# Kernel optimization log

Measured on AMD Instinct MI355X. Metric: run time of the kernel, lower is better.

## Reference

```python
import jax, jax.numpy as jnp
import numpy as np

D = 128  # hard-coded hidden dim in MLP_T

def setup_inputs() -> dict:
    key = jax.random.key(0)
    ks = jax.random.split(key, 8)
    N, IN = 16384, 768
    return {
        "x": jax.random.normal(ks[0], (N, IN), dtype=jnp.float32),
        "decay_value": 1,
        "W_token": jax.random.normal(ks[1], (IN, D), dtype=jnp.float32) * (IN ** -0.5),
        "b_token": jax.random.normal(ks[2], (D,), dtype=jnp.float32) * 0.02,
        "W_qkv": jax.random.normal(ks[3], (D, 3 * D), dtype=jnp.float32) * (D ** -0.5),
        "b_qkv": jax.random.normal(ks[4], (3 * D,), dtype=jnp.float32) * 0.02,
        "W_fc": jax.random.normal(ks[5], (D, 1), dtype=jnp.float32) * (D ** -0.5),
        "b_fc": jax.random.normal(ks[6], (1,), dtype=jnp.float32) * 0.02,
    }

def reference(x, decay_value, W_token, b_token, W_qkv, b_qkv, W_fc, b_fc):
    # token projection: [N, in_chan] -> [N, 128]
    h = x @ W_token + b_token
    # qkv: [N, 384] split along feature dim into q, k, v of [N, 128]
    qkv = h @ W_qkv + b_qkv
    q, k, v = qkv[:, :D], qkv[:, D:2 * D], qkv[:, 2 * D:]
    # sigmoid attention (no row normalization); dropout is identity in eval mode
    att_scores = jax.nn.sigmoid(q @ k.T)            # [N, N]
    att = att_scores @ v                            # [N, 128]
    out = att @ W_fc + b_fc                         # [N, 1]
    # GradientReversal is identity in the forward pass
    return out
```

## Files before the change

### kernel.cpp

```cpp
#include <hip/hip_runtime.h>
#include <hip/hip_bf16.h>
#include <stdint.h>

#define N_ROWS 16384

typedef __bf16 bf16x8 __attribute__((ext_vector_type(8)));
typedef float f32x4 __attribute__((ext_vector_type(4)));

#define AS1 __attribute__((address_space(1)))
#define AS3 __attribute__((address_space(3)))

#define OFF_WCP  0u
#define OFF_BC   589824u
#define OFF_QB   591360u
#define OFF_KB   4785664u
#define OFF_WV   8979968u
#define OFF_PART 9045504u

__global__ void prep(const float* __restrict__ Wt, const float* __restrict__ Wq,
                     const float* __restrict__ bt, const float* __restrict__ bq,
                     __bf16* __restrict__ WcP, float* __restrict__ bc) {
    int u = blockIdx.x * 256 + threadIdx.x;
    if (u < 768 * 96) {
        int k = u / 96, n4 = u % 96;
        float s[4] = {0, 0, 0, 0};
        const float* wtp = Wt + k * 128;
        const float* wqp = Wq + n4 * 4;
#pragma unroll 8
        for (int d = 0; d < 128; d++) {
            float a = wtp[d];
            float4 b = *(const float4*)(wqp + d * 384);
            s[0] += a * b.x; s[1] += a * b.y; s[2] += a * b.z; s[3] += a * b.w;
        }
        int kbi = k >> 6, j = (k >> 3) & 7, k7 = k & 7;
#pragma unroll
        for (int jj = 0; jj < 4; jj++) {
            int n = n4 * 4 + jj;
            int sr = n >> 1, b = n & 1;
            WcP[kbi * 24576 + sr * 128 + (b * 8 + (j ^ (sr & 7))) * 8 + k7] = (__bf16)s[jj];
        }
    }
    if (u < 384) {
        float s = bq[u];
        for (int d = 0; d < 128; d++) s += bt[d] * Wq[d * 384 + u];
        bc[u] = s;
    }
}

__launch_bounds__(128)
__global__ void gemm_qkv(const float* __restrict__ x, const __bf16* __restrict__ WcP,
                         const float* __restrict__ bc, const float* __restrict__ W_fc,
                         __bf16* __restrict__ qb, __bf16* __restrict__ kb,
                         float* __restrict__ wv) {
    __shared__ float  Asm_[32 * 64];
    __shared__ __bf16 Bsm[384 * 64];
    const int tid = threadIdx.x, wave = tid >> 6, lane = tid & 63;
    const int n16 = lane & 15, q = lane >> 4;
    const int row0 = blockIdx.x * 32;

    const char* asrc[4];
#pragma unroll
    for (int ii = 0; ii < 4; ii++) {
        int r = wave * 16 + ii * 4 + (lane >> 4);
        int cp = lane & 15;
        int c = 2 * ((cp >> 1) ^ (r & 7)) + ((cp & 1) ^ ((r >> 3) & 1));
        asrc[ii] = (const char*)(x + (size_t)(row0 + r) * 768 + c * 4);
    }
    const char* bsrc = (const char*)WcP + (size_t)wave * 24576 + lane * 16;

    f32x4 acc[24];
#pragma unroll
    for (int t = 0; t < 24; t++) acc[t] = (f32x4){0, 0, 0, 0};

    const int rA = wave * 16 + n16;
    const int sa = rA & 7, hb = (rA >> 3) & 1;
    const int bbase = (n16 >> 1) * 256 + (n16 & 1) * 128;
    const int sb = (n16 >> 1) & 7;

    for (int kbi = 0; kbi < 12; kbi++) {
#pragma unroll
        for (int ii = 0; ii < 4; ii++)
            __builtin_amdgcn_global_load_lds((const AS1 void*)(asrc[ii] + kbi * 256),
                (AS3 void*)((char*)Asm_ + (wave * 4 + ii) * 1024 + lane * 16), 16, 0, 0);
#pragma unroll
        for (int ii = 0; ii < 24; ii++)
            __builtin_amdgcn_global_load_lds((const AS1 void*)(bsrc + (size_t)kbi * 49152 + ii * 1024),
                (AS3 void*)((char*)Bsm + (wave * 24 + ii) * 1024 + lane * 16), 16, 0, 0);
        __syncthreads();
#pragma unroll
        for (int ksub = 0; ksub < 2; ksub++) {
            const int P = ksub * 4 + q;
            const float* ap = Asm_ + rA * 64;
            f32x4 f0 = *(const f32x4*)(ap + (2 * (P ^ sa) + hb) * 4);
            f32x4 f1 = *(const f32x4*)(ap + (2 * (P ^ sa) + (1 ^ hb)) * 4);
            bf16x8 af;
            af[0] = (__bf16)f0[0]; af[1] = (__bf16)f0[1]; af[2] = (__bf16)f0[2]; af[3] = (__bf16)f0[3];
            af[4] = (__bf16)f1[0]; af[5] = (__bf16)f1[1]; af[6] = (__bf16)f1[2]; af[7] = (__bf16)f1[3];
            const char* bp = (const char*)Bsm + bbase + (P ^ sb) * 16 - (n16 & 1) * 128
                             + (n16 & 1) * 128;
            (void)bp;
#pragma unroll
            for (int t = 0; t < 24; t++) {
                const char* bpt = (const char*)Bsm + (n16 >> 1) * 256
                                  + ((n16 & 1) * 8 + (P ^ sb)) * 16 + t * 2048;
                bf16x8 bf = *(const bf16x8*)bpt;
                acc[t] = __builtin_amdgcn_mfma_f32_16x16x32_bf16(af, bf, acc[t], 0, 0, 0);
            }
        }
        __syncthreads();
    }

    float wacc[4] = {0, 0, 0, 0};
#pragma unroll
    for (int t = 0; t < 24; t++) {
        int col = t * 16 + n16;
        float bcv = bc[col];
        float wf = (t >= 16) ? W_fc[col - 256] : 0.0f;
#pragma unroll
        for (int r = 0; r < 4; r++) {
            int row = row0 + wave * 16 + q * 4 + r;
            float val = acc[t][r] + bcv;
            if (t < 8) {
                qb[row * 128 + col] = (__bf16)(val * -1.44269504088896f);
            } else if (t < 16) {
                int d = col - 128;
                kb[row * 128 + (((d >> 3) ^ (row & 15)) << 3) + (d & 7)] = (__bf16)val;
            } else {
                wacc[r] += val * wf;
            }
        }
    }
#pragma unroll
    for (int r = 0; r < 4; r++) {
        float v = wacc[r];
        v += __shfl_xor(v, 1, 64);
        v += __shfl_xor(v, 2, 64);
        v += __shfl_xor(v, 4, 64);
        v += __shfl_xor(v, 8, 64);
        if (n16 == 0) wv[row0 + wave * 16 + q * 4 + r] = v;
    }
}

__launch_bounds__(128)
__global__ void attn(const __bf16* __restrict__ qb, const __bf16* __restrict__ kb,
                     const float* __restrict__ wv, float* __restrict__ partial) {
    __shared__ __bf16 kbuf[64 * 128];
    __shared__ float wbuf[64];
    const int tid = threadIdx.x;
    const int wave = tid >> 6, lane = tid & 63;
    const int n16 = lane & 15, q = lane >> 4;
    const int row0 = blockIdx.x * 128 + wave * 64;
    const int sp = blockIdx.y;
    bf16x8 qf[4][4];
#pragma unroll
    for (int mt = 0; mt < 4; mt++)
#pragma unroll
        for (int ks = 0; ks < 4; ks++)
            qf[mt][ks] = *(const bf16x8*)(qb + (row0 + mt * 16 + n16) * 128 + ks * 32 + q * 8);
    float acc[4][4] = {{0}, {0}, {0}, {0}};
    for (int jc = 0; jc < 16; jc++) {
        const int jbase = sp * 1024 + jc * 64;
        const char* gsrc = (const char*)kb + (size_t)jbase * 256;
#pragma unroll
        for (int i = 0; i < 8; i++) {
            const int off = wave * 8192 + i * 1024;
            __builtin_amdgcn_global_load_lds(
                (const AS1 void*)(gsrc + off + lane * 16),
                (AS3 void*)((char*)kbuf + off), 16, 0, 0);
        }
        if (tid < 64) wbuf[tid] = wv[jbase + tid];
        __syncthreads();
#pragma unroll
        for (int t = 0; t < 4; t++) {
            f32x4 s[4];
#pragma unroll
            for (int mt = 0; mt < 4; mt++) s[mt] = (f32x4){0, 0, 0, 0};
#pragma unroll
            for (int ks = 0; ks < 4; ks++) {
                const int chunk = (ks * 4 + q) ^ n16;
                bf16x8 bf = *(const bf16x8*)(kbuf + (t * 16 + n16) * 128 + chunk * 8);
#pragma unroll
                for (int mt = 0; mt < 4; mt++)
                    s[mt] = __builtin_amdgcn_mfma_f32_16x16x32_bf16(qf[mt][ks], bf, s[mt], 0, 0, 0);
            }
            const float wval = wbuf[t * 16 + n16];
#pragma unroll
            for (int mt = 0; mt < 4; mt++)
#pragma unroll
                for (int r = 0; r < 4; r++)
                    acc[mt][r] += __builtin_amdgcn_rcpf(1.0f + __builtin_amdgcn_exp2f(s[mt][r])) * wval;
        }
        __syncthreads();
    }
#pragma unroll
    for (int mt = 0; mt < 4; mt++)
#pragma unroll
        for (int r = 0; r < 4; r++) {
            float v = acc[mt][r];
            v += __shfl_xor(v, 1, 64);
            v += __shfl_xor(v, 2, 64);
            v += __shfl_xor(v, 4, 64);
            v += __shfl_xor(v, 8, 64);
            if (n16 == 0) partial[sp * N_ROWS + row0 + mt * 16 + q * 4 + r] = v;
        }
}

__global__ void reduce_out(const float* __restrict__ partial, const float* __restrict__ b_fc,
                           float* __restrict__ out) {
    int i = blockIdx.x * 256 + threadIdx.x;
    float v = b_fc[0];
#pragma unroll
    for (int s = 0; s < 16; s++) v += partial[s * N_ROWS + i];
    out[i] = v;
}

extern "C" void kernel_launch(void* const* d_in, const int* in_sizes, int n_in,
                              void* d_out, int out_size, void* d_ws, size_t ws_size,
                              hipStream_t stream) {
    const float* x       = (const float*)d_in[0];
    const float* W_token = (const float*)d_in[2];
    const float* b_token = (const float*)d_in[3];
    const float* W_qkv   = (const float*)d_in[4];
    const float* b_qkv   = (const float*)d_in[5];
    const float* W_fc    = (const float*)d_in[6];
    const float* b_fc    = (const float*)d_in[7];
    float* out = (float*)d_out;
    char* ws = (char*)d_ws;

    __bf16* WcP = (__bf16*)(ws + OFF_WCP);
    float*  bc  = (float*)(ws + OFF_BC);
    __bf16* qb  = (__bf16*)(ws + OFF_QB);
    __bf16* kb  = (__bf16*)(ws + OFF_KB);
    float*  wv  = (float*)(ws + OFF_WV);
    float*  part = (float*)(ws + OFF_PART);

    prep<<<288, 256, 0, stream>>>(W_token, W_qkv, b_token, b_qkv, WcP, bc);
    gemm_qkv<<<512, 128, 0, stream>>>(x, WcP, bc, W_fc, qb, kb, wv);
    attn<<<dim3(128, 16), 128, 0, stream>>>(qb, kb, wv, part);
    reduce_out<<<64, 256, 0, stream>>>(part, b_fc, out);
}
```

Measured before the change: 230.3 us.

## Retile QKV GEMM with double buffering, enlarge attention tiles, replace reduce with atomics

The QKV GEMM now uses 256-thread blocks over 64 rows, with each wave owning 96 output columns. It double-buffers the A and B tiles in LDS so the next k-block loads while the current one computes. The attention kernel doubles both the per-wave query tile (128 rows) and the key chunk (128 keys), so each loaded K fragment feeds 8 MFMAs. The 16 split partials are now combined with atomicAdd into the output, which the GEMM kernel pre-initializes with b_fc, removing the separate reduce launch and partial buffer. Risks are higher register pressure in attention (qf[8][4] plus 8 accumulators, with launch bounds of 2 blocks), fewer blocks in both kernels, and nondeterministic float atomic ordering.

```diff
diff --git a/kernel.cpp b/kernel.cpp
--- a/kernel.cpp
+++ b/kernel.cpp
@@ -15,7 +15,6 @@
 #define OFF_QB   591360u
 #define OFF_KB   4785664u
 #define OFF_WV   8979968u
-#define OFF_PART 9045504u
 
 __global__ void prep(const float* __restrict__ Wt, const float* __restrict__ Wq,
                      const float* __restrict__ bt, const float* __restrict__ bq,
@@ -47,153 +46,191 @@
     }
 }
 
-__launch_bounds__(128)
+__launch_bounds__(256)
 __global__ void gemm_qkv(const float* __restrict__ x, const __bf16* __restrict__ WcP,
                          const float* __restrict__ bc, const float* __restrict__ W_fc,
+                         const float* __restrict__ b_fc,
                          __bf16* __restrict__ qb, __bf16* __restrict__ kb,
-                         float* __restrict__ wv) {
-    __shared__ float  Asm_[32 * 64];
-    __shared__ __bf16 Bsm[384 * 64];
+                         float* __restrict__ wv, float* __restrict__ out) {
+    __shared__ float  Asm_[2][64 * 64];
+    __shared__ __bf16 Bsm[2][24576];
+    __shared__ float  wred[2][64];
     const int tid = threadIdx.x, wave = tid >> 6, lane = tid & 63;
     const int n16 = lane & 15, q = lane >> 4;
-    const int row0 = blockIdx.x * 32;
-
-    const char* asrc[4];
-#pragma unroll
-    for (int ii = 0; ii < 4; ii++) {
-        int r = wave * 16 + ii * 4 + (lane >> 4);
-        int cp = lane & 15;
-        int c = 2 * ((cp >> 1) ^ (r & 7)) + ((cp & 1) ^ ((r >> 3) & 1));
-        asrc[ii] = (const char*)(x + (size_t)(row0 + r) * 768 + c * 4);
-    }
-    const char* bsrc = (const char*)WcP + (size_t)wave * 24576 + lane * 16;
-
-    f32x4 acc[24];
-#pragma unroll
-    for (int t = 0; t < 24; t++) acc[t] = (f32x4){0, 0, 0, 0};
-
-    const int rA = wave * 16 + n16;
-    const int sa = rA & 7, hb = (rA >> 3) & 1;
-    const int bbase = (n16 >> 1) * 256 + (n16 & 1) * 128;
-    const int sb = (n16 >> 1) & 7;
-
+    const int row0 = blockIdx.x * 64;
+
+    if (tid < 64) out[row0 + tid] = b_fc[0];
+
+    const char* aptr[4];
+#pragma unroll
+    for (int i = 0; i < 4; i++) {
+        int ar = row0 + wave * 16 + i * 4 + (lane >> 4);
+        int p = (lane & 15) >> 1, half = lane & 1;
+        aptr[i] = (const char*)x + (size_t)ar * 3072 + ((p ^ (ar & 7)) * 8 + half * 4) * 4;
+    }
+    const char* bsrc = (const char*)WcP + (size_t)wave * 12288 + lane * 16;
+
+    f32x4 acc[4][6];
+#pragma unroll
+    for (int mt = 0; mt < 4; mt++)
+#pragma unroll
+        for (int tt = 0; tt < 6; tt++) acc[mt][tt] = (f32x4){0, 0, 0, 0};
+
+#define STAGE(KBI, BUF)                                                                  \
+    do {                                                                                 \
+        _Pragma("unroll")                                                                \
+        for (int i = 0; i < 4; i++)                                                      \
+            __builtin_amdgcn_global_load_lds((const AS1 void*)(aptr[i] + (KBI) * 256),   \
+                (AS3 void*)((char*)Asm_[BUF] + wave * 4096 + i * 1024), 16, 0, 0);       \
+        _Pragma("unroll")                                                                \
+        for (int i = 0; i < 12; i++)                                                     \
+            __builtin_amdgcn_global_load_lds(                                            \
+                (const AS1 void*)(bsrc + (size_t)(KBI) * 49152 + i * 1024),              \
+                (AS3 void*)((char*)Bsm[BUF] + wave * 12288 + i * 1024), 16, 0, 0);       \
+    } while (0)
+
+    STAGE(0, 0);
     for (int kbi = 0; kbi < 12; kbi++) {
-#pragma unroll
-        for (int ii = 0; ii < 4; ii++)
-            __builtin_amdgcn_global_load_lds((const AS1 void*)(asrc[ii] + kbi * 256),
-                (AS3 void*)((char*)Asm_ + (wave * 4 + ii) * 1024 + lane * 16), 16, 0, 0);
-#pragma unroll
-        for (int ii = 0; ii < 24; ii++)
-            __builtin_amdgcn_global_load_lds((const AS1 void*)(bsrc + (size_t)kbi * 49152 + ii * 1024),
-                (AS3 void*)((char*)Bsm + (wave * 24 + ii) * 1024 + lane * 16), 16, 0, 0);
+        const int cur = kbi & 1;
         __syncthreads();
-#pragma unroll
-        for (int ksub = 0; ksub < 2; ksub++) {
-            const int P = ksub * 4 + q;
-            const float* ap = Asm_ + rA * 64;
-            f32x4 f0 = *(const f32x4*)(ap + (2 * (P ^ sa) + hb) * 4);
-            f32x4 f1 = *(const f32x4*)(ap + (2 * (P ^ sa) + (1 ^ hb)) * 4);
-            bf16x8 af;
-            af[0] = (__bf16)f0[0]; af[1] = (__bf16)f0[1]; af[2] = (__bf16)f0[2]; af[3] = (__bf16)f0[3];
-            af[4] = (__bf16)f1[0]; af[5] = (__bf16)f1[1]; af[6] = (__bf16)f1[2]; af[7] = (__bf16)f1[3];
-            const char* bp = (const char*)Bsm + bbase + (P ^ sb) * 16 - (n16 & 1) * 128
-                             + (n16 & 1) * 128;
-            (void)bp;
-#pragma unroll
-            for (int t = 0; t < 24; t++) {
-                const char* bpt = (const char*)Bsm + (n16 >> 1) * 256
-                                  + ((n16 & 1) * 8 + (P ^ sb)) * 16 + t * 2048;
+        if (kbi + 1 < 12) STAGE(kbi + 1, cur ^ 1);
+        const float* Ab = Asm_[cur];
+        const char* Bb = (const char*)Bsm[cur];
+#pragma unroll
+        for (int ks = 0; ks < 2; ks++) {
+            const int P = ks * 4 + q;
+            bf16x8 af[4];
+#pragma unroll
+            for (int mt = 0; mt < 4; mt++) {
+                const int r = mt * 16 + n16;
+                const int sa = r & 7;
+                const float* ap = Ab + r * 64 + ((P ^ sa) << 3);
+                f32x4 f0 = *(const f32x4*)ap;
+                f32x4 f1 = *(const f32x4*)(ap + 4);
+                bf16x8 t;
+                t[0] = (__bf16)f0[0]; t[1] = (__bf16)f0[1]; t[2] = (__bf16)f0[2]; t[3] = (__bf16)f0[3];
+                t[4] = (__bf16)f1[0]; t[5] = (__bf16)f1[1]; t[6] = (__bf16)f1[2]; t[7] = (__bf16)f1[3];
+                af[mt] = t;
+            }
+#pragma unroll
+            for (int tt = 0; tt < 6; tt++) {
+                const char* bpt = Bb + (wave * 48 + tt * 8 + (n16 >> 1)) * 256
+                                  + ((n16 & 1) * 8 + (P ^ (n16 >> 1))) * 16;
                 bf16x8 bf = *(const bf16x8*)bpt;
-                acc[t] = __builtin_amdgcn_mfma_f32_16x16x32_bf16(af, bf, acc[t], 0, 0, 0);
-            }
-        }
-        __syncthreads();
-    }
-
-    float wacc[4] = {0, 0, 0, 0};
-#pragma unroll
-    for (int t = 0; t < 24; t++) {
-        int col = t * 16 + n16;
-        float bcv = bc[col];
-        float wf = (t >= 16) ? W_fc[col - 256] : 0.0f;
-#pragma unroll
-        for (int r = 0; r < 4; r++) {
-            int row = row0 + wave * 16 + q * 4 + r;
-            float val = acc[t][r] + bcv;
-            if (t < 8) {
-                qb[row * 128 + col] = (__bf16)(val * -1.44269504088896f);
-            } else if (t < 16) {
-                int d = col - 128;
-                kb[row * 128 + (((d >> 3) ^ (row & 15)) << 3) + (d & 7)] = (__bf16)val;
-            } else {
-                wacc[r] += val * wf;
-            }
-        }
-    }
-#pragma unroll
-    for (int r = 0; r < 4; r++) {
-        float v = wacc[r];
-        v += __shfl_xor(v, 1, 64);
-        v += __shfl_xor(v, 2, 64);
-        v += __shfl_xor(v, 4, 64);
-        v += __shfl_xor(v, 8, 64);
-        if (n16 == 0) wv[row0 + wave * 16 + q * 4 + r] = v;
-    }
-}
-
-__launch_bounds__(128)
+#pragma unroll
+                for (int mt = 0; mt < 4; mt++)
+                    acc[mt][tt] = __builtin_amdgcn_mfma_f32_16x16x32_bf16(af[mt], bf, acc[mt][tt], 0, 0, 0);
+            }
+        }
+    }
+#undef STAGE
+
+    float wacc[4][4] = {{0}, {0}, {0}, {0}};
+#pragma unroll
+    for (int tt = 0; tt < 6; tt++) {
+        const int c0 = wave * 96 + tt * 16;
+        const int col = c0 + n16;
+        const float bcv = bc[col];
+        if (c0 < 128) {
+#pragma unroll
+            for (int mt = 0; mt < 4; mt++)
+#pragma unroll
+                for (int rr = 0; rr < 4; rr++) {
+                    int row = row0 + mt * 16 + q * 4 + rr;
+                    qb[row * 128 + col] = (__bf16)((acc[mt][tt][rr] + bcv) * -1.44269504088896f);
+                }
+        } else if (c0 < 256) {
+            const int d = col - 128;
+#pragma unroll
+            for (int mt = 0; mt < 4; mt++)
+#pragma unroll
+                for (int rr = 0; rr < 4; rr++) {
+                    int row = row0 + mt * 16 + q * 4 + rr;
+                    kb[row * 128 + (((d >> 3) ^ (row & 15)) << 3) + (d & 7)] = (__bf16)(acc[mt][tt][rr] + bcv);
+                }
+        } else {
+            const float wf = W_fc[col - 256];
+#pragma unroll
+            for (int mt = 0; mt < 4; mt++)
+#pragma unroll
+                for (int rr = 0; rr < 4; rr++) wacc[mt][rr] += (acc[mt][tt][rr] + bcv) * wf;
+        }
+    }
+    if (wave >= 2) {
+#pragma unroll
+        for (int mt = 0; mt < 4; mt++)
+#pragma unroll
+            for (int rr = 0; rr < 4; rr++) {
+                float v = wacc[mt][rr];
+                v += __shfl_xor(v, 1, 64);
+                v += __shfl_xor(v, 2, 64);
+                v += __shfl_xor(v, 4, 64);
+                v += __shfl_xor(v, 8, 64);
+                if (n16 == 0) wred[wave - 2][mt * 16 + q * 4 + rr] = v;
+            }
+    }
+    __syncthreads();
+    if (tid < 64) wv[row0 + tid] = wred[0][tid] + wred[1][tid];
+}
+
+__launch_bounds__(128, 2)
 __global__ void attn(const __bf16* __restrict__ qb, const __bf16* __restrict__ kb,
-                     const float* __restrict__ wv, float* __restrict__ partial) {
-    __shared__ __bf16 kbuf[64 * 128];
-    __shared__ float wbuf[64];
+                     const float* __restrict__ wv, float* __restrict__ out) {
+    __shared__ __bf16 kbuf[128 * 128];
+    __shared__ float wbuf[128];
     const int tid = threadIdx.x;
     const int wave = tid >> 6, lane = tid & 63;
     const int n16 = lane & 15, q = lane >> 4;
-    const int row0 = blockIdx.x * 128 + wave * 64;
+    const int row0 = blockIdx.x * 256 + wave * 128;
     const int sp = blockIdx.y;
-    bf16x8 qf[4][4];
-#pragma unroll
-    for (int mt = 0; mt < 4; mt++)
+
+    bf16x8 qf[8][4];
+#pragma unroll
+    for (int mt = 0; mt < 8; mt++)
 #pragma unroll
         for (int ks = 0; ks < 4; ks++)
             qf[mt][ks] = *(const bf16x8*)(qb + (row0 + mt * 16 + n16) * 128 + ks * 32 + q * 8);
-    float acc[4][4] = {{0}, {0}, {0}, {0}};
-    for (int jc = 0; jc < 16; jc++) {
-        const int jbase = sp * 1024 + jc * 64;
+
+    float acc[8][4] = {{0}, {0}, {0}, {0}, {0}, {0}, {0}, {0}};
+    for (int jc = 0; jc < 8; jc++) {
+        const int jbase = sp * 1024 + jc * 128;
         const char* gsrc = (const char*)kb + (size_t)jbase * 256;
 #pragma unroll
-        for (int i = 0; i < 8; i++) {
-            const int off = wave * 8192 + i * 1024;
+        for (int i = 0; i < 16; i++) {
+            const int off = wave * 16384 + i * 1024;
             __builtin_amdgcn_global_load_lds(
                 (const AS1 void*)(gsrc + off + lane * 16),
                 (AS3 void*)((char*)kbuf + off), 16, 0, 0);
         }
-        if (tid < 64) wbuf[tid] = wv[jbase + tid];
+        wbuf[tid] = wv[jbase + tid];
         __syncthreads();
 #pragma unroll
-        for (int t = 0; t < 4; t++) {
-            f32x4 s[4];
-#pragma unroll
-            for (int mt = 0; mt < 4; mt++) s[mt] = (f32x4){0, 0, 0, 0};
+        for (int t = 0; t < 8; t++) {
+            bf16x8 bf[4];
 #pragma unroll
             for (int ks = 0; ks < 4; ks++) {
                 const int chunk = (ks * 4 + q) ^ n16;
-                bf16x8 bf = *(const bf16x8*)(kbuf + (t * 16 + n16) * 128 + chunk * 8);
-#pragma unroll
-                for (int mt = 0; mt < 4; mt++)
-                    s[mt] = __builtin_amdgcn_mfma_f32_16x16x32_bf16(qf[mt][ks], bf, s[mt], 0, 0, 0);
-            }
+                bf[ks] = *(const bf16x8*)(kbuf + (t * 16 + n16) * 128 + chunk * 8);
+            }
+            f32x4 sc[8];
+#pragma unroll
+            for (int mt = 0; mt < 8; mt++) sc[mt] = (f32x4){0, 0, 0, 0};
+#pragma unroll
+            for (int ks = 0; ks < 4; ks++)
+#pragma unroll
+                for (int mt = 0; mt < 8; mt++)
+                    sc[mt] = __builtin_amdgcn_mfma_f32_16x16x32_bf16(qf[mt][ks], bf[ks], sc[mt], 0, 0, 0);
             const float wval = wbuf[t * 16 + n16];
 #pragma unroll
-            for (int mt = 0; mt < 4; mt++)
+            for (int mt = 0; mt < 8; mt++)
 #pragma unroll
                 for (int r = 0; r < 4; r++)
-                    acc[mt][r] += __builtin_amdgcn_rcpf(1.0f + __builtin_amdgcn_exp2f(s[mt][r])) * wval;
+                    acc[mt][r] += __builtin_amdgcn_rcpf(1.0f + __builtin_amdgcn_exp2f(sc[mt][r])) * wval;
         }
         __syncthreads();
     }
 #pragma unroll
-    for (int mt = 0; mt < 4; mt++)
+    for (int mt = 0; mt < 8; mt++)
 #pragma unroll
         for (int r = 0; r < 4; r++) {
             float v = acc[mt][r];
@@ -201,17 +238,8 @@
             v += __shfl_xor(v, 2, 64);
             v += __shfl_xor(v, 4, 64);
             v += __shfl_xor(v, 8, 64);
-            if (n16 == 0) partial[sp * N_ROWS + row0 + mt * 16 + q * 4 + r] = v;
-        }
-}
-
-__global__ void reduce_out(const float* __restrict__ partial, const float* __restrict__ b_fc,
-                           float* __restrict__ out) {
-    int i = blockIdx.x * 256 + threadIdx.x;
-    float v = b_fc[0];
-#pragma unroll
-    for (int s = 0; s < 16; s++) v += partial[s * N_ROWS + i];
-    out[i] = v;
+            if (n16 == 0) atomicAdd(&out[row0 + mt * 16 + q * 4 + r], v);
+        }
 }
 
 extern "C" void kernel_launch(void* const* d_in, const int* in_sizes, int n_in,
@@ -232,10 +260,8 @@
     __bf16* qb  = (__bf16*)(ws + OFF_QB);
     __bf16* kb  = (__bf16*)(ws + OFF_KB);
     float*  wv  = (float*)(ws + OFF_WV);
-    float*  part = (float*)(ws + OFF_PART);
 
     prep<<<288, 256, 0, stream>>>(W_token, W_qkv, b_token, b_qkv, WcP, bc);
-    gemm_qkv<<<512, 128, 0, stream>>>(x, WcP, bc, W_fc, qb, kb, wv);
-    attn<<<dim3(128, 16), 128, 0, stream>>>(qb, kb, wv, part);
-    reduce_out<<<64, 256, 0, stream>>>(part, b_fc, out);
-}
+    gemm_qkv<<<256, 256, 0, stream>>>(x, WcP, bc, W_fc, b_fc, qb, kb, wv, out);
+    attn<<<dim3(64, 16), 128, 0, stream>>>(qb, kb, wv, out);
+}
```

New measurement: 748.5 us. 225% more time.
